# Kernel optimization log

Measured on AMD Instinct MI355X. Metric: run time of the kernel, lower is better.

## Reference

```python
import jax, jax.numpy as jnp
import numpy as np

B, H, S, D, HID = 2, 4, 512, 16, 32

def setup_inputs() -> dict:
    key = jax.random.key(0)
    ks = jax.random.split(key, 12)
    sc = 1.0 / np.sqrt(D)
    return {
        "v": jax.random.normal(ks[0], (B, H, S, D), jnp.float32),
        "k": jax.random.normal(ks[1], (B, H, S, D), jnp.float32),
        "q": jax.random.normal(ks[2], (B, H, S, D), jnp.float32),
        "mask": jnp.zeros((B, 1, S, S), jnp.float32),
        "Wq": jax.random.normal(ks[3], (D, D), jnp.float32) * sc,
        "bq": jnp.zeros((D,), jnp.float32),
        "Wk": jax.random.normal(ks[4], (D, D), jnp.float32) * sc,
        "bk": jnp.zeros((D,), jnp.float32),
        "Wv": jax.random.normal(ks[5], (D, D), jnp.float32) * sc,
        "bv": jnp.zeros((D,), jnp.float32),
        "Wo": jax.random.normal(ks[6], (D, D), jnp.float32) * sc,
        "bo": jnp.zeros((D,), jnp.float32),
        "N1": jax.random.normal(ks[7], (2 * D, HID), jnp.float32) * (1.0 / np.sqrt(2 * D)),
        "b1": jnp.zeros((HID,), jnp.float32),
        "N2": jax.random.normal(ks[8], (HID, 1), jnp.float32) * (1.0 / np.sqrt(HID)),
        "b2": jnp.zeros((1,), jnp.float32),
    }

def _pair_mlp_scores(qh, kh, N1, b1, N2, b2):
    # NN(concat(q_i, k_j)) computed without materializing the 2*D concat:
    # first layer = q_i @ N1[:D] + k_j @ N1[D:] + b1, broadcast-summed over pairs.
    d = qh.shape[-1]
    A, Bm = N1[:d], N1[d:]
    hq = jnp.einsum("bhsd,df->bhsf", qh, A)   # (B,H,Sq,HID)
    hk = jnp.einsum("bhsd,df->bhsf", kh, Bm)  # (B,H,Sk,HID)
    pre = hq[:, :, :, None, :] + hk[:, :, None, :, :] + b1  # (B,H,Sq,Sk,HID)
    return jnp.einsum("bhqkf,fo->bhqk", jax.nn.relu(pre), N2[:, :]) + b2[0]

def reference(v, k, q, mask, Wq, bq, Wk, bk, Wv, bv, Wo, bo, N1, b1, N2, b2):
    qp = q @ Wq + bq
    kp = k @ Wk + bk
    vp = v @ Wv + bv
    logits = _pair_mlp_scores(qp, kp, N1, b1, N2, b2)
    # make_sym=True: add NN(concat(k_j, q_i))
    logits = logits + _pair_mlp_scores(kp, qp, N1, b1, N2, b2).swapaxes(-1, -2)
    logits = logits + mask * -1e9
    attn = jax.nn.softmax(logits, axis=-1)          # (B,H,Sq,Sk)
    out = jnp.einsum("bhqk,bhkd->bhqd", attn, vp)   # (B,H,Sq,D)
    return out @ Wo + bo, attn
```

## Files before the change

### kernel.cpp

```cpp
#include <hip/hip_runtime.h>

#define NB 2
#define NH 4
#define NS 512
#define ND 16
#define NF 32

typedef float v2f __attribute__((ext_vector_type(2)));


__global__ __launch_bounds__(256) void k_proj(
    const float* __restrict__ q, const float* __restrict__ kin, const float* __restrict__ v,
    const float* __restrict__ Wq, const float* __restrict__ bq,
    const float* __restrict__ Wk, const float* __restrict__ bk,
    const float* __restrict__ Wv, const float* __restrict__ bv,
    const float* __restrict__ N1, const float* __restrict__ b1,
    float* __restrict__ hq_rm, float* __restrict__ hk, float* __restrict__ vpt)
{
    __shared__ float m_s[16 * 32];
    __shared__ float c_s[32];
    __shared__ float trans_s[256 * 33];

    const int bid = blockIdx.x;
    const int job = bid % 5;
    const int sc  = (bid / 5) & 1;
    const int bh  = bid / 10;
    const int t   = threadIdx.x;

    const float* W    = (job < 2) ? Wq : (job < 4 ? Wk : Wv);
    const float* bias = (job < 2) ? bq : (job < 4 ? bk : bv);
    const float* x    = (job < 2) ? q  : (job < 4 ? kin : v);

    if (job < 4) {
        const int noff = (job & 1) * 16;
        for (int i = t; i < 512; i += 256) {
            int e = i >> 5, f = i & 31;
            float m = 0.f;
#pragma unroll
            for (int d = 0; d < 16; ++d)
                m = fmaf(W[e * 16 + d], N1[(noff + d) * 32 + f], m);
            m_s[i] = m;
        }
        if (t < 32) {
            float c = (job & 1) ? b1[t] : 0.f;
#pragma unroll
            for (int d = 0; d < 16; ++d)
                c = fmaf(bias[d], N1[(noff + d) * 32 + t], c);
            c_s[t] = c;
        }
    } else {
        int e = t >> 4, d = t & 15;
        m_s[e * 32 + d] = W[e * 16 + d];
        if (t < 16) c_s[t] = bias[t];
    }
    __syncthreads();

    const int s = sc * 256 + t;
    const int r = bh * NS + s;

    float xv[16];
    const float4* x4 = (const float4*)(x + (size_t)r * 16);
#pragma unroll
    for (int j = 0; j < 4; ++j) {
        float4 a = x4[j];
        xv[4*j] = a.x; xv[4*j+1] = a.y; xv[4*j+2] = a.z; xv[4*j+3] = a.w;
    }

    if (job < 2) {
        float h[32];
#pragma unroll
        for (int f = 0; f < 32; ++f) h[f] = c_s[f];
#pragma unroll
        for (int e = 0; e < 16; ++e)
#pragma unroll
            for (int f = 0; f < 32; ++f)
                h[f] = fmaf(xv[e], m_s[e * 32 + f], h[f]);
#pragma unroll
        for (int f = 0; f < 32; ++f) trans_s[t * 33 + f] = h[f];
        __syncthreads();
        float* outb = hq_rm + (((size_t)(bh * NS + sc * 256)) << 6) + (job & 1) * 32;
#pragma unroll
        for (int it = 0; it < 32; ++it) {
            int j = it * 256 + t;
            int sl = j >> 5, f = j & 31;
            outb[((size_t)sl << 6) + f] = trans_s[sl * 33 + f];
        }
    } else if (job < 4) {
        float* outb = hk + (size_t)bh * 32768 + (size_t)(job & 1) * 16384;
        float h[32];
#pragma unroll
        for (int f = 0; f < 32; ++f) h[f] = c_s[f];
#pragma unroll
        for (int e = 0; e < 16; ++e)
#pragma unroll
            for (int f = 0; f < 32; ++f)
                h[f] = fmaf(xv[e], m_s[e * 32 + f], h[f]);
#pragma unroll
        for (int f = 0; f < 32; ++f)
            outb[(size_t)f * NS + s] = h[f];
    } else {
        float* outb = vpt + (size_t)bh * 8192;
        float h[16];
#pragma unroll
        for (int d = 0; d < 16; ++d) h[d] = c_s[d];
#pragma unroll
        for (int e = 0; e < 16; ++e)
#pragma unroll
            for (int d = 0; d < 16; ++d)
                h[d] = fmaf(xv[e], m_s[e * 32 + d], h[d]);
#pragma unroll
        for (int d = 0; d < 16; ++d)
            outb[(size_t)d * NS + s] = h[d];
    }
}

__global__ __launch_bounds__(512, 4) void k_fused(
    const float* __restrict__ hq_rm, const float* __restrict__ hk,
    const float* __restrict__ vpt,
    const float* __restrict__ N2, const float* __restrict__ b2,
    const float* __restrict__ mask,
    const float* __restrict__ Wo, const float* __restrict__ bo,
    float* __restrict__ attn, float* __restrict__ out)
{
    __shared__ __align__(16) float attn_s[8 * 516];
    __shared__ float wo_s[256];
    __shared__ float bo_s[16];
    __shared__ float ov_s[128];
    __shared__ float part_s[128 * 17];
    __shared__ float redm[64];
    __shared__ float reds[64];

    const int bh  = blockIdx.x >> 6;
    const int q0  = (blockIdx.x & 63) << 3;
    const int tid = threadIdx.x;
    const int wave = tid >> 6, lane = tid & 63;
    const int k = tid;
    const size_t base = (size_t)bh * 32768;

    v2f hk2A[16], hk2B[16], n2v[16];
#pragma unroll
    for (int f2 = 0; f2 < 16; ++f2) {
        hk2A[f2] = (v2f){ hk[base + (size_t)(2*f2    ) * NS + k],
                          hk[base + (size_t)(2*f2 + 1) * NS + k] };
        hk2B[f2] = (v2f){ hk[base + (size_t)(32 + 2*f2) * NS + k],
                          hk[base + (size_t)(33 + 2*f2) * NS + k] };
        n2v[f2]  = (v2f){ N2[2*f2], N2[2*f2 + 1] };
    }
    const float b2v = 2.0f * b2[0];
    const float* mbase = mask + (size_t)(bh >> 2) * NS * NS;

    if (tid < 256) wo_s[tid] = Wo[tid];
    if (tid < 16)  bo_s[tid] = bo[tid];
    __syncthreads();

    float sreg[8];
    float mnext = mbase[(size_t)q0 * NS + k];
#pragma unroll
    for (int qi = 0; qi < 8; ++qi) {
        float mcur = mnext;
        if (qi < 7) mnext = mbase[(size_t)(q0 + qi + 1) * NS + k];
        const v2f* hq2 = (const v2f*)(hq_rm + (((size_t)(bh * NS + q0 + qi)) << 6));
        v2f acc_a = 0.f, acc_b = 0.f;
        const v2f z = 0.f;
#pragma unroll
        for (int f2 = 0; f2 < 16; ++f2) {
            v2f t1 = hq2[f2]      + hk2B[f2];
            v2f t2 = hq2[16 + f2] + hk2A[f2];
            v2f r  = __builtin_elementwise_max(t1, z) + __builtin_elementwise_max(t2, z);
            if (f2 & 1) acc_b += n2v[f2] * r;
            else        acc_a += n2v[f2] * r;
        }
        v2f av = acc_a + acc_b;
        float s = av.x + av.y + b2v;
        s = fmaf(mcur, -1e9f, s);
        sreg[qi] = s;

        float m = s;
#pragma unroll
        for (int off = 32; off > 0; off >>= 1) m = fmaxf(m, __shfl_xor(m, off));
        if (lane == 0) redm[qi * 8 + wave] = m;
    }
    __syncthreads();

    float preg[8];
#pragma unroll
    for (int qi = 0; qi < 8; ++qi) {
        float bm = redm[qi * 8];
#pragma unroll
        for (int w = 1; w < 8; ++w) bm = fmaxf(bm, redm[qi * 8 + w]);
        float e = __expf(sreg[qi] - bm);
        preg[qi] = e;
        float ss = e;
#pragma unroll
        for (int off = 32; off > 0; off >>= 1) ss += __shfl_xor(ss, off);
        if (lane == 0) reds[qi * 8 + wave] = ss;
    }
    __syncthreads();

#pragma unroll
    for (int qi = 0; qi < 8; ++qi) {
        float tot = reds[qi * 8];
#pragma unroll
        for (int w = 1; w < 8; ++w) tot += reds[qi * 8 + w];
        float p = preg[qi] / tot;
        attn[(size_t)(bh * NS + q0 + qi) * NS + k] = p;
        attn_s[qi * 516 + k] = p;
    }
    __syncthreads();

    {
        const int qi_p = tid & 7;
        const int dgrp = (tid >> 3) & 3;
        const int koct = tid >> 5;
        const float4* a4 = (const float4*)attn_s;
        const float4* v4 = (const float4*)(vpt + (size_t)bh * 8192);
        float acc0 = 0.f, acc1 = 0.f, acc2 = 0.f, acc3 = 0.f;
#pragma unroll
        for (int kq = 0; kq < 8; ++kq) {
            const int k4 = koct * 8 + kq;
            float4 av = a4[qi_p * 129 + k4];
            float4 w0 = v4[(dgrp * 4 + 0) * 128 + k4];
            float4 w1 = v4[(dgrp * 4 + 1) * 128 + k4];
            float4 w2 = v4[(dgrp * 4 + 2) * 128 + k4];
            float4 w3 = v4[(dgrp * 4 + 3) * 128 + k4];
            acc0 = fmaf(av.x, w0.x, fmaf(av.y, w0.y, fmaf(av.z, w0.z, fmaf(av.w, w0.w, acc0))));
            acc1 = fmaf(av.x, w1.x, fmaf(av.y, w1.y, fmaf(av.z, w1.z, fmaf(av.w, w1.w, acc1))));
            acc2 = fmaf(av.x, w2.x, fmaf(av.y, w2.y, fmaf(av.z, w2.z, fmaf(av.w, w2.w, acc2))));
            acc3 = fmaf(av.x, w3.x, fmaf(av.y, w3.y, fmaf(av.z, w3.z, fmaf(av.w, w3.w, acc3))));
        }
        part_s[(qi_p * 16 + dgrp * 4 + 0) * 17 + koct] = acc0;
        part_s[(qi_p * 16 + dgrp * 4 + 1) * 17 + koct] = acc1;
        part_s[(qi_p * 16 + dgrp * 4 + 2) * 17 + koct] = acc2;
        part_s[(qi_p * 16 + dgrp * 4 + 3) * 17 + koct] = acc3;
    }
    __syncthreads();

    if (tid < 128) {
        float ov = 0.f;
#pragma unroll
        for (int kh = 0; kh < 16; ++kh) ov += part_s[tid * 17 + kh];
        ov_s[tid] = ov;
    }
    __syncthreads();

    if (tid < 128) {
        const int qi2 = tid >> 4, d = tid & 15;
        float res = bo_s[d];
#pragma unroll
        for (int e = 0; e < 16; ++e)
            res = fmaf(ov_s[qi2 * 16 + e], wo_s[e * 16 + d], res);
        out[(size_t)(bh * NS + q0 + qi2) * 16 + d] = res;
    }
}

extern "C" void kernel_launch(void* const* d_in, const int* in_sizes, int n_in,
                              void* d_out, int out_size, void* d_ws, size_t ws_size,
                              hipStream_t stream)
{
    const float* v    = (const float*)d_in[0];
    const float* k    = (const float*)d_in[1];
    const float* q    = (const float*)d_in[2];
    const float* mask = (const float*)d_in[3];
    const float* Wq   = (const float*)d_in[4];
    const float* bq   = (const float*)d_in[5];
    const float* Wk   = (const float*)d_in[6];
    const float* bk   = (const float*)d_in[7];
    const float* Wv   = (const float*)d_in[8];
    const float* bv   = (const float*)d_in[9];
    const float* Wo   = (const float*)d_in[10];
    const float* bo   = (const float*)d_in[11];
    const float* N1   = (const float*)d_in[12];
    const float* b1   = (const float*)d_in[13];
    const float* N2   = (const float*)d_in[14];
    const float* b2   = (const float*)d_in[15];

    float* out  = (float*)d_out;
    float* attn = out + (size_t)NB*NH*NS*ND;

    float* hq_rm = (float*)d_ws;
    float* hk    = hq_rm + (size_t)8 * 32768;
    float* vpt   = hk + (size_t)8 * 32768;

    k_proj <<<80, 256, 0, stream>>>(q, k, v, Wq, bq, Wk, bk, Wv, bv, N1, b1, hq_rm, hk, vpt);
    k_fused<<<512, 512, 0, stream>>>(hq_rm, hk, vpt, N2, b2, mask, Wo, bo, attn, out);
}
```

Baseline: 32.96 us.

## Pack hk as float4 per key, vectorize pair-MLP and use single-pass online softmax

The k-projection output moves from a feature-major layout to a packed layout of four features per key, so the fused kernel loads hk with float4 reads and runs the pair-MLP on 4-wide vectors. The softmax now takes each wave's local max and exp-sum in one pass and combines them across waves with a rescale, which removes a full block barrier and a second round of shuffles. The mask values are prefetched into registers up front, and the division becomes a reciprocal multiply. This costs extra exp calls during the merge and adds small numerical differences from rcp and the rescaling.

```diff
diff --git a/kernel.cpp b/kernel.cpp
--- a/kernel.cpp
+++ b/kernel.cpp
@@ -6,7 +6,7 @@
 #define ND 16
 #define NF 32
 
-typedef float v2f __attribute__((ext_vector_type(2)));
+typedef float v4f __attribute__((ext_vector_type(4)));
 
 
 __global__ __launch_bounds__(256) void k_proj(
@@ -15,7 +15,7 @@
     const float* __restrict__ Wk, const float* __restrict__ bk,
     const float* __restrict__ Wv, const float* __restrict__ bv,
     const float* __restrict__ N1, const float* __restrict__ b1,
-    float* __restrict__ hq_rm, float* __restrict__ hk, float* __restrict__ vpt)
+    float* __restrict__ hq_rm, float* __restrict__ hkp, float* __restrict__ vpt)
 {
     __shared__ float m_s[16 * 32];
     __shared__ float c_s[32];
@@ -66,7 +66,7 @@
         xv[4*j] = a.x; xv[4*j+1] = a.y; xv[4*j+2] = a.z; xv[4*j+3] = a.w;
     }
 
-    if (job < 2) {
+    if (job < 4) {
         float h[32];
 #pragma unroll
         for (int f = 0; f < 32; ++f) h[f] = c_s[f];
@@ -78,26 +78,25 @@
 #pragma unroll
         for (int f = 0; f < 32; ++f) trans_s[t * 33 + f] = h[f];
         __syncthreads();
-        float* outb = hq_rm + (((size_t)(bh * NS + sc * 256)) << 6) + (job & 1) * 32;
-#pragma unroll
-        for (int it = 0; it < 32; ++it) {
-            int j = it * 256 + t;
-            int sl = j >> 5, f = j & 31;
-            outb[((size_t)sl << 6) + f] = trans_s[sl * 33 + f];
-        }
-    } else if (job < 4) {
-        float* outb = hk + (size_t)bh * 32768 + (size_t)(job & 1) * 16384;
-        float h[32];
-#pragma unroll
-        for (int f = 0; f < 32; ++f) h[f] = c_s[f];
-#pragma unroll
-        for (int e = 0; e < 16; ++e)
-#pragma unroll
-            for (int f = 0; f < 32; ++f)
-                h[f] = fmaf(xv[e], m_s[e * 32 + f], h[f]);
-#pragma unroll
-        for (int f = 0; f < 32; ++f)
-            outb[(size_t)f * NS + s] = h[f];
+
+        if (job < 2) {
+            float* outb = hq_rm + (((size_t)(bh * NS + sc * 256)) << 6) + (job & 1) * 32;
+#pragma unroll
+            for (int it = 0; it < 32; ++it) {
+                int j = it * 256 + t;
+                int sl = j >> 5, f = j & 31;
+                outb[((size_t)sl << 6) + f] = trans_s[sl * 33 + f];
+            }
+        } else {
+            float* outb = hkp + (size_t)bh * 32768 + (size_t)(job & 1) * 16384 + sc * 1024;
+#pragma unroll
+            for (int it = 0; it < 32; ++it) {
+                int i = it * 256 + t;
+                int f4 = i >> 10, rem = i & 1023;
+                int sl = rem >> 2, c = rem & 3;
+                outb[(size_t)f4 * 2048 + rem] = trans_s[sl * 33 + f4 * 4 + c];
+            }
+        }
     } else {
         float* outb = vpt + (size_t)bh * 8192;
         float h[16];
@@ -115,7 +114,7 @@
 }
 
 __global__ __launch_bounds__(512, 4) void k_fused(
-    const float* __restrict__ hq_rm, const float* __restrict__ hk,
+    const float* __restrict__ hq_rm, const float* __restrict__ hkp,
     const float* __restrict__ vpt,
     const float* __restrict__ N2, const float* __restrict__ b2,
     const float* __restrict__ mask,
@@ -137,72 +136,67 @@
     const int k = tid;
     const size_t base = (size_t)bh * 32768;
 
-    v2f hk2A[16], hk2B[16], n2v[16];
-#pragma unroll
-    for (int f2 = 0; f2 < 16; ++f2) {
-        hk2A[f2] = (v2f){ hk[base + (size_t)(2*f2    ) * NS + k],
-                          hk[base + (size_t)(2*f2 + 1) * NS + k] };
-        hk2B[f2] = (v2f){ hk[base + (size_t)(32 + 2*f2) * NS + k],
-                          hk[base + (size_t)(33 + 2*f2) * NS + k] };
-        n2v[f2]  = (v2f){ N2[2*f2], N2[2*f2 + 1] };
-    }
+    v4f hkA4[8], hkB4[8];
+    const v4f* hkb = (const v4f*)(hkp + base + (size_t)k * 4);
+#pragma unroll
+    for (int f4 = 0; f4 < 8; ++f4) hkA4[f4] = hkb[f4 * 512];
+#pragma unroll
+    for (int f4 = 0; f4 < 8; ++f4) hkB4[f4] = hkb[4096 + f4 * 512];
+
+    v4f n24[8];
+#pragma unroll
+    for (int f4 = 0; f4 < 8; ++f4)
+        n24[f4] = (v4f){ N2[4*f4], N2[4*f4+1], N2[4*f4+2], N2[4*f4+3] };
     const float b2v = 2.0f * b2[0];
+
     const float* mbase = mask + (size_t)(bh >> 2) * NS * NS;
+    float mreg[8];
+#pragma unroll
+    for (int qi = 0; qi < 8; ++qi) mreg[qi] = mbase[(size_t)(q0 + qi) * NS + k];
 
     if (tid < 256) wo_s[tid] = Wo[tid];
     if (tid < 16)  bo_s[tid] = bo[tid];
     __syncthreads();
 
     float sreg[8];
-    float mnext = mbase[(size_t)q0 * NS + k];
 #pragma unroll
     for (int qi = 0; qi < 8; ++qi) {
-        float mcur = mnext;
-        if (qi < 7) mnext = mbase[(size_t)(q0 + qi + 1) * NS + k];
-        const v2f* hq2 = (const v2f*)(hq_rm + (((size_t)(bh * NS + q0 + qi)) << 6));
-        v2f acc_a = 0.f, acc_b = 0.f;
-        const v2f z = 0.f;
-#pragma unroll
-        for (int f2 = 0; f2 < 16; ++f2) {
-            v2f t1 = hq2[f2]      + hk2B[f2];
-            v2f t2 = hq2[16 + f2] + hk2A[f2];
-            v2f r  = __builtin_elementwise_max(t1, z) + __builtin_elementwise_max(t2, z);
-            if (f2 & 1) acc_b += n2v[f2] * r;
-            else        acc_a += n2v[f2] * r;
-        }
-        v2f av = acc_a + acc_b;
-        float s = av.x + av.y + b2v;
-        s = fmaf(mcur, -1e9f, s);
-        sreg[qi] = s;
+        const v4f* hq4 = (const v4f*)(hq_rm + (((size_t)(bh * NS + q0 + qi)) << 6));
+        v4f acc = 0.f;
+        const v4f z = 0.f;
+#pragma unroll
+        for (int f4 = 0; f4 < 8; ++f4) {
+            v4f t1 = hq4[f4]     + hkB4[f4];
+            v4f t2 = hq4[8 + f4] + hkA4[f4];
+            v4f rr = __builtin_elementwise_max(t1, z) + __builtin_elementwise_max(t2, z);
+            acc += n24[f4] * rr;
+        }
+        float s = (acc.x + acc.y) + (acc.z + acc.w) + b2v;
+        s = fmaf(mreg[qi], -1e9f, s);
 
         float m = s;
 #pragma unroll
         for (int off = 32; off > 0; off >>= 1) m = fmaxf(m, __shfl_xor(m, off));
-        if (lane == 0) redm[qi * 8 + wave] = m;
-    }
-    __syncthreads();
-
-    float preg[8];
+        float e = __expf(s - m);
+        sreg[qi] = s - m;
+        float ss = e;
+#pragma unroll
+        for (int off = 32; off > 0; off >>= 1) ss += __shfl_xor(ss, off);
+        if (lane == 0) { redm[qi * 8 + wave] = m; reds[qi * 8 + wave] = ss; }
+    }
+    __syncthreads();
+
 #pragma unroll
     for (int qi = 0; qi < 8; ++qi) {
-        float bm = redm[qi * 8];
-#pragma unroll
-        for (int w = 1; w < 8; ++w) bm = fmaxf(bm, redm[qi * 8 + w]);
-        float e = __expf(sreg[qi] - bm);
-        preg[qi] = e;
-        float ss = e;
-#pragma unroll
-        for (int off = 32; off > 0; off >>= 1) ss += __shfl_xor(ss, off);
-        if (lane == 0) reds[qi * 8 + wave] = ss;
-    }
-    __syncthreads();
-
-#pragma unroll
-    for (int qi = 0; qi < 8; ++qi) {
-        float tot = reds[qi * 8];
-#pragma unroll
-        for (int w = 1; w < 8; ++w) tot += reds[qi * 8 + w];
-        float p = preg[qi] / tot;
+        float M = redm[qi * 8];
+#pragma unroll
+        for (int w = 1; w < 8; ++w) M = fmaxf(M, redm[qi * 8 + w]);
+        float tot = 0.f;
+#pragma unroll
+        for (int w = 0; w < 8; ++w)
+            tot = fmaf(reds[qi * 8 + w], __expf(redm[qi * 8 + w] - M), tot);
+        float mw = redm[qi * 8 + wave];
+        float p = __expf(sreg[qi] + (mw - M)) * __builtin_amdgcn_rcpf(tot);
         attn[(size_t)(bh * NS + q0 + qi) * NS + k] = p;
         attn_s[qi * 516 + k] = p;
     }
@@ -278,9 +272,9 @@
     float* attn = out + (size_t)NB*NH*NS*ND;
 
     float* hq_rm = (float*)d_ws;
-    float* hk    = hq_rm + (size_t)8 * 32768;
-    float* vpt   = hk + (size_t)8 * 32768;
-
-    k_proj <<<80, 256, 0, stream>>>(q, k, v, Wq, bq, Wk, bk, Wv, bv, N1, b1, hq_rm, hk, vpt);
-    k_fused<<<512, 512, 0, stream>>>(hq_rm, hk, vpt, N2, b2, mask, Wo, bo, attn, out);
+    float* hkp   = hq_rm + (size_t)8 * 32768;
+    float* vpt   = hkp + (size_t)8 * 32768;
+
+    k_proj <<<80, 256, 0, stream>>>(q, k, v, Wq, bq, Wk, bk, Wv, bv, N1, b1, hq_rm, hkp, vpt);
+    k_fused<<<512, 512, 0, stream>>>(hq_rm, hkp, vpt, N2, b2, mask, Wo, bo, attn, out);
 }
```

After: 32.14 us. 2.5% less time.
